# Performance work log

Measured on AMD Instinct MI355X. Metric: run time of the kernel, lower is better.

## Reference

```python
import jax, jax.numpy as jnp
import numpy as np

B, D, P = 8192, 256, 4096
TEMP = 0.5
MOMENTUM = 0.9
EPS = 1e-12  # matches torch F.normalize eps


def _l2_normalize(x):
    n = jnp.sqrt(jnp.sum(x * x, axis=1, keepdims=True))
    return x / jnp.maximum(n, EPS)


def setup_inputs() -> dict:
    key = jax.random.key(0)
    k1, k2, k3 = jax.random.split(key, 3)
    embeddings = jax.random.normal(k1, (B, D), dtype=jnp.float32)
    prototypes = jax.random.normal(k2, (P, D), dtype=jnp.float32)
    cluster_ids = jax.random.randint(k3, (B,), 0, P, dtype=jnp.int64)
    return {"embeddings": embeddings, "prototypes": prototypes, "cluster_ids": cluster_ids}


def reference(embeddings, prototypes, cluster_ids):
    cluster_ids = cluster_ids.astype(jnp.int32)
    emb_norm = _l2_normalize(embeddings)            # [B, D]
    proto_norm = _l2_normalize(prototypes)          # [P, D]
    sim = (emb_norm @ proto_norm.T) / TEMP          # [B, P]

    rows = jnp.arange(sim.shape[0])
    pos_sim = sim[rows, cluster_ids]                # [B]
    neg_sim = sim.at[rows, cluster_ids].set(-jnp.inf)
    # stable logsumexp over negatives (positive column masked out)
    max_val = jnp.max(neg_sim, axis=1, keepdims=True)
    lse = jnp.log(jnp.sum(jnp.exp(neg_sim - max_val), axis=1)) + max_val[:, 0]
    loss = jnp.mean(-pos_sim + lse)

    # serial per-sample EMA prototype update (faithful to the torch for-loop,
    # including sequential dependence on repeated cluster ids)
    def step(protos, xe):
        cid, e = xe
        new_row = MOMENTUM * protos[cid] + (1.0 - MOMENTUM) * e
        return protos.at[cid].set(new_row), None

    new_prototypes, _ = jax.lax.scan(step, prototypes, (cluster_ids, embeddings))
    return loss, new_prototypes
```

## Files before the change

kernel.cpp:

```cpp
#include <hip/hip_runtime.h>
#include <hip/hip_bf16.h>
#include <math.h>

#define Bn 8192
#define Dn 256
#define Pn 4096

using f16x8 = _Float16 __attribute__((ext_vector_type(8)));
using f16x4 = _Float16 __attribute__((ext_vector_type(4)));
using f32x16 = float __attribute__((ext_vector_type(16)));

__global__ void norm_hist_kernel(const float* __restrict__ emb, const float* __restrict__ protos,
                                 const int* __restrict__ cid,
                                 _Float16* __restrict__ embn, _Float16* __restrict__ pron,
                                 float* __restrict__ s_glob, int* __restrict__ hist) {
    __shared__ int h[Pn];
    int gid  = blockIdx.x;
    bool do_hist = (gid < Bn / 256);
    if (do_hist)
        for (int c = threadIdx.x; c < Pn; c += 256) h[c] = 0;

    int row  = gid * 4 + (threadIdx.x >> 6);
    int lane = threadIdx.x & 63;
    const float* in;
    _Float16* out;
    int r;
    if (row < Bn) { in = emb;    out = embn; r = row; }
    else          { in = protos; out = pron; r = row - Bn; }
    const float4 v = reinterpret_cast<const float4*>(in + (size_t)r * Dn)[lane];
    float ss = v.x * v.x + v.y * v.y + v.z * v.z + v.w * v.w;
#pragma unroll
    for (int m = 1; m <= 32; m <<= 1) ss += __shfl_xor(ss, m);
    float scale = 1.0f / fmaxf(sqrtf(ss), 1e-12f);
    f16x4 o;
    o[0] = (_Float16)(v.x * scale);
    o[1] = (_Float16)(v.y * scale);
    o[2] = (_Float16)(v.z * scale);
    o[3] = (_Float16)(v.w * scale);
    reinterpret_cast<f16x4*>(out + (size_t)r * Dn)[lane] = o;

    if (gid < Bn / 1024) s_glob[gid * 256 + threadIdx.x] = 0.0f;

    if (do_hist) {
        __syncthreads();
        atomicAdd(&h[cid[gid * 256 + threadIdx.x]], 1);
        __syncthreads();
        for (int c = threadIdx.x; c < Pn; c += 256)
            hist[gid * Pn + c] = h[c];
    }
}

__global__ __launch_bounds__(1024)
void prefscan_kernel(const int* __restrict__ hist, int* __restrict__ pref,
                     int* __restrict__ offs) {
    __shared__ int wt[16];
    int t = threadIdx.x;
    int4 run = {0, 0, 0, 0};
    for (int ch = 0; ch < 32; ++ch) {
        int4 v = reinterpret_cast<const int4*>(hist + ch * Pn)[t];
        reinterpret_cast<int4*>(pref + ch * Pn)[t] = run;
        run.x += v.x; run.y += v.y; run.z += v.z; run.w += v.w;
    }
    int l1 = run.x, l2 = l1 + run.y, l3 = l2 + run.z;
    int tot = l3 + run.w;
    int v = tot;
#pragma unroll
    for (int d = 1; d < 64; d <<= 1) {
        int u = __shfl_up(v, d);
        if ((t & 63) >= d) v += u;
    }
    if ((t & 63) == 63) wt[t >> 6] = v;
    __syncthreads();
    int add = 0;
    for (int ww = 0; ww < (t >> 6); ++ww) add += wt[ww];
    int base = add + v - tot;
    int4 o = {base, base + l1, base + l2, base + l3};
    reinterpret_cast<int4*>(offs)[t] = o;
    if (t == 0) offs[Pn] = Bn;
}

__global__ void rankfill_kernel(const int* __restrict__ cid, const int* __restrict__ pref,
                                const int* __restrict__ offs, int* __restrict__ slist) {
    __shared__ int ids[256];
    int t = threadIdx.x, g = blockIdx.x;
    int i = g * 256 + t;
    int my = cid[i];
    ids[t] = my;
    __syncthreads();
    int r = pref[g * Pn + my];
    for (int j = 0; j < t; ++j) r += (ids[j] == my) ? 1 : 0;
    slist[offs[my] + r] = i;
}

__global__ __launch_bounds__(256, 2)
void gemm_expsum_kernel(const _Float16* __restrict__ embn, const _Float16* __restrict__ pron,
                        const int* __restrict__ cid,
                        float* __restrict__ s_glob, float* __restrict__ pos_glob) {
    __shared__ _Float16 Bs[2][32 * Dn];
    const int w    = threadIdx.x >> 6;
    const int lane = threadIdx.x & 63;
    const int lo   = lane & 31;
    const int hi   = lane >> 5;
    const int rbase = blockIdx.x * 128 + w * 32;
    const int cbase = blockIdx.y * 256;

    const _Float16* ap = embn + (size_t)(rbase + lo) * Dn + hi * 8;
    f16x8 a[16];
#pragma unroll
    for (int kk = 0; kk < 16; ++kk)
        a[kk] = *reinterpret_cast<const f16x8*>(ap + kk * 16);

    int cidr[16];
#pragma unroll
    for (int r = 0; r < 16; ++r)
        cidr[r] = cid[rbase + (r & 3) + 8 * (r >> 2) + 4 * hi];

    float s[16];
#pragma unroll
    for (int r = 0; r < 16; ++r) s[r] = 0.0f;

    constexpr float K1 = 2.0f * 1.4426950408889634f;

    auto stage = [&](int sub, _Float16* buf) {
#pragma unroll
        for (int i = 0; i < 4; ++i) {
            int g = i * 4 + w;
            const _Float16* gsrc =
                pron + (size_t)(cbase + sub * 32 + lo) * Dn + g * 16 + hi * 8;
            char* l = (char*)buf + (g << 10);
            __builtin_amdgcn_global_load_lds(
                (const __attribute__((address_space(1))) unsigned int*)gsrc,
                (__attribute__((address_space(3))) unsigned int*)l, 16, 0, 0);
        }
    };

    stage(0, Bs[0]);
    __syncthreads();

    for (int sub = 0; sub < 8; ++sub) {
        const _Float16* cur = Bs[sub & 1];
        if (sub < 7) stage(sub + 1, Bs[(sub + 1) & 1]);

        f32x16 acc;
#pragma unroll
        for (int r = 0; r < 16; ++r) acc[r] = 0.0f;
#pragma unroll
        for (int kk = 0; kk < 16; ++kk) {
            f16x8 b = *reinterpret_cast<const f16x8*>(
                (const char*)cur + (kk << 10) + (lane << 4));
            acc = __builtin_amdgcn_mfma_f32_32x32x16_f16(a[kk], b, acc, 0, 0, 0);
        }
        int colv = cbase + sub * 32 + lo;
#pragma unroll
        for (int r = 0; r < 16; ++r) {
            float e = exp2f(fmaf(acc[r], K1, -K1));
            bool ispos = (cidr[r] == colv);
            s[r] += ispos ? 0.0f : e;
            if (ispos)
                pos_glob[rbase + (r & 3) + 8 * (r >> 2) + 4 * hi] = acc[r] * 2.0f;
        }
        __syncthreads();
    }

#pragma unroll
    for (int r = 0; r < 16; ++r) {
        float v = s[r];
        v += __shfl_xor(v, 1);
        v += __shfl_xor(v, 2);
        v += __shfl_xor(v, 4);
        v += __shfl_xor(v, 8);
        v += __shfl_xor(v, 16);
        if (lo == 0) {
            int row = rbase + (r & 3) + 8 * (r >> 2) + 4 * hi;
            atomicAdd(&s_glob[row], v);
        }
    }
}

__global__ void update_loss_kernel(const float* __restrict__ protos, const float* __restrict__ emb,
                                   const int* __restrict__ offs, const int* __restrict__ slist,
                                   const float* __restrict__ s_glob, const float* __restrict__ pos_glob,
                                   float* __restrict__ out) {
    __shared__ float ws2[4];
    float* outp = out + 1;
    int w = threadIdx.x >> 6, lane = threadIdx.x & 63;
    int c = blockIdx.x * 4 + w;
    int off = offs[c], cnt = offs[c + 1] - off;
    float4 p = reinterpret_cast<const float4*>(protos + (size_t)c * Dn)[lane];
    float scale = __powf(0.9f, (float)cnt);
    float4 acc;
    acc.x = p.x * scale; acc.y = p.y * scale; acc.z = p.z * scale; acc.w = p.w * scale;
    for (int j = 0; j < cnt; ++j) {
        int i = slist[off + j];
        float wgt = 0.1f * __powf(0.9f, (float)(cnt - 1 - j));
        float4 e = reinterpret_cast<const float4*>(emb + (size_t)i * Dn)[lane];
        acc.x += wgt * e.x; acc.y += wgt * e.y; acc.z += wgt * e.z; acc.w += wgt * e.w;
    }
    reinterpret_cast<float4*>(outp + (size_t)c * Dn)[lane] = acc;

    if (blockIdx.x == 0) {
        float ssum = 0.0f;
        for (int i = threadIdx.x; i < Bn; i += 256)
            ssum += __logf(s_glob[i]) + 2.0f - pos_glob[i];
#pragma unroll
        for (int m = 1; m <= 32; m <<= 1) ssum += __shfl_xor(ssum, m);
        if ((threadIdx.x & 63) == 0) ws2[threadIdx.x >> 6] = ssum;
        __syncthreads();
        if (threadIdx.x == 0)
            out[0] = (ws2[0] + ws2[1] + ws2[2] + ws2[3]) * (1.0f / (float)Bn);
    }
}

extern "C" void kernel_launch(void* const* d_in, const int* in_sizes, int n_in,
                              void* d_out, int out_size, void* d_ws, size_t ws_size,
                              hipStream_t stream) {
    const float* emb    = (const float*)d_in[0];
    const float* protos = (const float*)d_in[1];
    const int*   cid    = (const int*)d_in[2];
    float* out = (float*)d_out;

    char* ws = (char*)d_ws;
    _Float16* embn = (_Float16*)ws;
    _Float16* pron = (_Float16*)(ws + ((size_t)4 << 20));
    float* s_glob  = (float*)(ws + ((size_t)6 << 20));
    float* pos_g   = (float*)(ws + ((size_t)6 << 20) + 32768);
    int*   offs    = (int*)(ws + ((size_t)6 << 20) + 65536);
    int*   slist   = (int*)(ws + ((size_t)6 << 20) + 98304);
    int*   hist    = (int*)(ws + ((size_t)7 << 20));
    int*   pref    = (int*)(ws + ((size_t)7 << 20) + 524288);

    norm_hist_kernel<<<(Bn + Pn) / 4, 256, 0, stream>>>(emb, protos, cid, embn, pron, s_glob, hist);
    prefscan_kernel<<<1, 1024, 0, stream>>>(hist, pref, offs);
    rankfill_kernel<<<Bn / 256, 256, 0, stream>>>(cid, pref, offs, slist);
    gemm_expsum_kernel<<<dim3(Bn / 128, Pn / 256), 256, 0, stream>>>(embn, pron, cid, s_glob, pos_g);
    update_loss_kernel<<<Pn / 4, 256, 0, stream>>>(protos, emb, offs, slist, s_glob, pos_g, out);
}
```

Measured before the change: 142.3 us.

## Fold softmax scale into embeddings and move positive-column handling out of GEMM

Pre-scales the normalized embeddings by 2/ln2 so the GEMM epilogue is a bare exp2 with no FMA, drops the per-element positive-column mask from the GEMM, and splits the K loop across two independent MFMA accumulators. A new small kernel recomputes the positive dot product, subtracts its exponential from the full sum and writes per-row loss terms. The single-block prefix scan is split into a parallel column-scan kernel and a small offsets kernel, with the GEMM launched earlier. Risks: dropping the max shift relies on bounded cosine similarities, subtracting the positive term can cancel catastrophically, and fp16 rounding of the scaled embedding changes precision slightly.

After: 145.5 us. +2.2%, slower.

```diff
diff --git a/kernel.cpp b/kernel.cpp
--- a/kernel.cpp
+++ b/kernel.cpp
@@ -5,6 +5,9 @@
 #define Bn 8192
 #define Dn 256
 #define Pn 4096
+
+#define SCALE 2.8853900817779268f
+#define LN2   0.6931471805599453f
 
 using f16x8 = _Float16 __attribute__((ext_vector_type(8)));
 using f16x4 = _Float16 __attribute__((ext_vector_type(4)));
@@ -25,13 +28,14 @@
     const float* in;
     _Float16* out;
     int r;
-    if (row < Bn) { in = emb;    out = embn; r = row; }
-    else          { in = protos; out = pron; r = row - Bn; }
+    float post;
+    if (row < Bn) { in = emb;    out = embn; r = row;      post = SCALE; }
+    else          { in = protos; out = pron; r = row - Bn; post = 1.0f;  }
     const float4 v = reinterpret_cast<const float4*>(in + (size_t)r * Dn)[lane];
     float ss = v.x * v.x + v.y * v.y + v.z * v.z + v.w * v.w;
 #pragma unroll
     for (int m = 1; m <= 32; m <<= 1) ss += __shfl_xor(ss, m);
-    float scale = 1.0f / fmaxf(sqrtf(ss), 1e-12f);
+    float scale = post / fmaxf(sqrtf(ss), 1e-12f);
     f16x4 o;
     o[0] = (_Float16)(v.x * scale);
     o[1] = (_Float16)(v.y * scale);
@@ -39,7 +43,7 @@
     o[3] = (_Float16)(v.w * scale);
     reinterpret_cast<f16x4*>(out + (size_t)r * Dn)[lane] = o;
 
-    if (gid < Bn / 1024) s_glob[gid * 256 + threadIdx.x] = 0.0f;
+    if (gid < 32) s_glob[gid * 256 + threadIdx.x] = 0.0f;
 
     if (do_hist) {
         __syncthreads();
@@ -50,32 +54,133 @@
     }
 }
 
-__global__ __launch_bounds__(1024)
-void prefscan_kernel(const int* __restrict__ hist, int* __restrict__ pref,
-                     int* __restrict__ offs) {
-    __shared__ int wt[16];
+__global__ __launch_bounds__(256, 2)
+void gemm_expsum_kernel(const _Float16* __restrict__ embn, const _Float16* __restrict__ pron,
+                        float* __restrict__ s_glob) {
+    __shared__ _Float16 Bs[2][32 * Dn];
+    const int w    = threadIdx.x >> 6;
+    const int lane = threadIdx.x & 63;
+    const int lo   = lane & 31;
+    const int hi   = lane >> 5;
+    const int rbase = blockIdx.x * 128 + w * 32;
+    const int cbase = blockIdx.y * 256;
+
+    const _Float16* ap = embn + (size_t)(rbase + lo) * Dn + hi * 8;
+    f16x8 a[16];
+#pragma unroll
+    for (int kk = 0; kk < 16; ++kk)
+        a[kk] = *reinterpret_cast<const f16x8*>(ap + kk * 16);
+
+    float s[16];
+#pragma unroll
+    for (int r = 0; r < 16; ++r) s[r] = 0.0f;
+
+    auto stage = [&](int sub, _Float16* buf) {
+#pragma unroll
+        for (int i = 0; i < 4; ++i) {
+            int g = i * 4 + w;
+            const _Float16* gsrc =
+                pron + (size_t)(cbase + sub * 32 + lo) * Dn + g * 16 + hi * 8;
+            char* l = (char*)buf + (g << 10);
+            __builtin_amdgcn_global_load_lds(
+                (const __attribute__((address_space(1))) unsigned int*)gsrc,
+                (__attribute__((address_space(3))) unsigned int*)l, 16, 0, 0);
+        }
+    };
+
+    stage(0, Bs[0]);
+    __syncthreads();
+
+    for (int sub = 0; sub < 8; ++sub) {
+        const _Float16* cur = Bs[sub & 1];
+        if (sub < 7) stage(sub + 1, Bs[(sub + 1) & 1]);
+
+        f32x16 acc0, acc1;
+#pragma unroll
+        for (int r = 0; r < 16; ++r) { acc0[r] = 0.0f; acc1[r] = 0.0f; }
+#pragma unroll
+        for (int kk = 0; kk < 16; kk += 2) {
+            f16x8 b0 = *reinterpret_cast<const f16x8*>(
+                (const char*)cur + (kk << 10) + (lane << 4));
+            acc0 = __builtin_amdgcn_mfma_f32_32x32x16_f16(a[kk], b0, acc0, 0, 0, 0);
+            f16x8 b1 = *reinterpret_cast<const f16x8*>(
+                (const char*)cur + ((kk + 1) << 10) + (lane << 4));
+            acc1 = __builtin_amdgcn_mfma_f32_32x32x16_f16(a[kk + 1], b1, acc1, 0, 0, 0);
+        }
+#pragma unroll
+        for (int r = 0; r < 16; ++r)
+            s[r] += exp2f(acc0[r] + acc1[r]);
+
+        __syncthreads();
+    }
+
+#pragma unroll
+    for (int r = 0; r < 16; ++r) {
+        float v = s[r];
+        v += __shfl_xor(v, 1);
+        v += __shfl_xor(v, 2);
+        v += __shfl_xor(v, 4);
+        v += __shfl_xor(v, 8);
+        v += __shfl_xor(v, 16);
+        if (lo == 0) {
+            int row = rbase + (r & 3) + 8 * (r >> 2) + 4 * hi;
+            atomicAdd(&s_glob[row], v);
+        }
+    }
+}
+
+__global__ void loss_terms_kernel(const _Float16* __restrict__ embn, const _Float16* __restrict__ pron,
+                                  const int* __restrict__ cid, const float* __restrict__ s_glob,
+                                  float* __restrict__ terms) {
+    int row  = blockIdx.x * 4 + (threadIdx.x >> 6);
+    int lane = threadIdx.x & 63;
+    int c = cid[row];
+    f16x4 e = reinterpret_cast<const f16x4*>(embn + (size_t)row * Dn)[lane];
+    f16x4 p = reinterpret_cast<const f16x4*>(pron + (size_t)c * Dn)[lane];
+    float d = 0.0f;
+#pragma unroll
+    for (int j = 0; j < 4; ++j) d += (float)e[j] * (float)p[j];
+#pragma unroll
+    for (int m = 1; m <= 32; m <<= 1) d += __shfl_xor(d, m);
+    if (lane == 0) {
+        float accp = d;
+        float sneg = s_glob[row] - exp2f(accp);
+        terms[row] = __logf(sneg) - LN2 * accp;
+    }
+}
+
+__global__ void counts_pref_kernel(const int* __restrict__ hist, int* __restrict__ counts,
+                                   int* __restrict__ pref) {
+    int c = blockIdx.x * 256 + threadIdx.x;
+    int s = 0;
+#pragma unroll
+    for (int ch = 0; ch < 32; ++ch) {
+        pref[ch * Pn + c] = s;
+        s += hist[ch * Pn + c];
+    }
+    counts[c] = s;
+}
+
+__global__ void offsets_kernel(const int* __restrict__ counts, int* __restrict__ offs) {
+    __shared__ int wtot[4];
     int t = threadIdx.x;
-    int4 run = {0, 0, 0, 0};
-    for (int ch = 0; ch < 32; ++ch) {
-        int4 v = reinterpret_cast<const int4*>(hist + ch * Pn)[t];
-        reinterpret_cast<int4*>(pref + ch * Pn)[t] = run;
-        run.x += v.x; run.y += v.y; run.z += v.z; run.w += v.w;
-    }
-    int l1 = run.x, l2 = l1 + run.y, l3 = l2 + run.z;
-    int tot = l3 + run.w;
-    int v = tot;
+    int local[16];
+    int run = 0;
+#pragma unroll
+    for (int j = 0; j < 16; ++j) { local[j] = run; run += counts[t * 16 + j]; }
+    int v = run;
 #pragma unroll
     for (int d = 1; d < 64; d <<= 1) {
         int u = __shfl_up(v, d);
         if ((t & 63) >= d) v += u;
     }
-    if ((t & 63) == 63) wt[t >> 6] = v;
+    if ((t & 63) == 63) wtot[t >> 6] = v;
     __syncthreads();
     int add = 0;
-    for (int ww = 0; ww < (t >> 6); ++ww) add += wt[ww];
-    int base = add + v - tot;
-    int4 o = {base, base + l1, base + l2, base + l3};
-    reinterpret_cast<int4*>(offs)[t] = o;
+    for (int ww = 0; ww < (t >> 6); ++ww) add += wtot[ww];
+    int excl = add + v - run;
+#pragma unroll
+    for (int j = 0; j < 16; ++j) offs[t * 16 + j] = excl + local[j];
     if (t == 0) offs[Pn] = Bn;
 }
 
@@ -92,95 +197,9 @@
     slist[offs[my] + r] = i;
 }
 
-__global__ __launch_bounds__(256, 2)
-void gemm_expsum_kernel(const _Float16* __restrict__ embn, const _Float16* __restrict__ pron,
-                        const int* __restrict__ cid,
-                        float* __restrict__ s_glob, float* __restrict__ pos_glob) {
-    __shared__ _Float16 Bs[2][32 * Dn];
-    const int w    = threadIdx.x >> 6;
-    const int lane = threadIdx.x & 63;
-    const int lo   = lane & 31;
-    const int hi   = lane >> 5;
-    const int rbase = blockIdx.x * 128 + w * 32;
-    const int cbase = blockIdx.y * 256;
-
-    const _Float16* ap = embn + (size_t)(rbase + lo) * Dn + hi * 8;
-    f16x8 a[16];
-#pragma unroll
-    for (int kk = 0; kk < 16; ++kk)
-        a[kk] = *reinterpret_cast<const f16x8*>(ap + kk * 16);
-
-    int cidr[16];
-#pragma unroll
-    for (int r = 0; r < 16; ++r)
-        cidr[r] = cid[rbase + (r & 3) + 8 * (r >> 2) + 4 * hi];
-
-    float s[16];
-#pragma unroll
-    for (int r = 0; r < 16; ++r) s[r] = 0.0f;
-
-    constexpr float K1 = 2.0f * 1.4426950408889634f;
-
-    auto stage = [&](int sub, _Float16* buf) {
-#pragma unroll
-        for (int i = 0; i < 4; ++i) {
-            int g = i * 4 + w;
-            const _Float16* gsrc =
-                pron + (size_t)(cbase + sub * 32 + lo) * Dn + g * 16 + hi * 8;
-            char* l = (char*)buf + (g << 10);
-            __builtin_amdgcn_global_load_lds(
-                (const __attribute__((address_space(1))) unsigned int*)gsrc,
-                (__attribute__((address_space(3))) unsigned int*)l, 16, 0, 0);
-        }
-    };
-
-    stage(0, Bs[0]);
-    __syncthreads();
-
-    for (int sub = 0; sub < 8; ++sub) {
-        const _Float16* cur = Bs[sub & 1];
-        if (sub < 7) stage(sub + 1, Bs[(sub + 1) & 1]);
-
-        f32x16 acc;
-#pragma unroll
-        for (int r = 0; r < 16; ++r) acc[r] = 0.0f;
-#pragma unroll
-        for (int kk = 0; kk < 16; ++kk) {
-            f16x8 b = *reinterpret_cast<const f16x8*>(
-                (const char*)cur + (kk << 10) + (lane << 4));
-            acc = __builtin_amdgcn_mfma_f32_32x32x16_f16(a[kk], b, acc, 0, 0, 0);
-        }
-        int colv = cbase + sub * 32 + lo;
-#pragma unroll
-        for (int r = 0; r < 16; ++r) {
-            float e = exp2f(fmaf(acc[r], K1, -K1));
-            bool ispos = (cidr[r] == colv);
-            s[r] += ispos ? 0.0f : e;
-            if (ispos)
-                pos_glob[rbase + (r & 3) + 8 * (r >> 2) + 4 * hi] = acc[r] * 2.0f;
-        }
-        __syncthreads();
-    }
-
-#pragma unroll
-    for (int r = 0; r < 16; ++r) {
-        float v = s[r];
-        v += __shfl_xor(v, 1);
-        v += __shfl_xor(v, 2);
-        v += __shfl_xor(v, 4);
-        v += __shfl_xor(v, 8);
-        v += __shfl_xor(v, 16);
-        if (lo == 0) {
-            int row = rbase + (r & 3) + 8 * (r >> 2) + 4 * hi;
-            atomicAdd(&s_glob[row], v);
-        }
-    }
-}
-
 __global__ void update_loss_kernel(const float* __restrict__ protos, const float* __restrict__ emb,
                                    const int* __restrict__ offs, const int* __restrict__ slist,
-                                   const float* __restrict__ s_glob, const float* __restrict__ pos_glob,
-                                   float* __restrict__ out) {
+                                   const float* __restrict__ terms, float* __restrict__ out) {
     __shared__ float ws2[4];
     float* outp = out + 1;
     int w = threadIdx.x >> 6, lane = threadIdx.x & 63;
@@ -200,8 +219,7 @@
 
     if (blockIdx.x == 0) {
         float ssum = 0.0f;
-        for (int i = threadIdx.x; i < Bn; i += 256)
-            ssum += __logf(s_glob[i]) + 2.0f - pos_glob[i];
+        for (int i = threadIdx.x; i < Bn; i += 256) ssum += terms[i];
 #pragma unroll
         for (int m = 1; m <= 32; m <<= 1) ssum += __shfl_xor(ssum, m);
         if ((threadIdx.x & 63) == 0) ws2[threadIdx.x >> 6] = ssum;
@@ -223,15 +241,18 @@
     _Float16* embn = (_Float16*)ws;
     _Float16* pron = (_Float16*)(ws + ((size_t)4 << 20));
     float* s_glob  = (float*)(ws + ((size_t)6 << 20));
-    float* pos_g   = (float*)(ws + ((size_t)6 << 20) + 32768);
+    float* terms   = (float*)(ws + ((size_t)6 << 20) + 32768);
     int*   offs    = (int*)(ws + ((size_t)6 << 20) + 65536);
     int*   slist   = (int*)(ws + ((size_t)6 << 20) + 98304);
+    int*   counts  = (int*)(ws + ((size_t)6 << 20) + 131072);
     int*   hist    = (int*)(ws + ((size_t)7 << 20));
     int*   pref    = (int*)(ws + ((size_t)7 << 20) + 524288);
 
     norm_hist_kernel<<<(Bn + Pn) / 4, 256, 0, stream>>>(emb, protos, cid, embn, pron, s_glob, hist);
-    prefscan_kernel<<<1, 1024, 0, stream>>>(hist, pref, offs);
+    gemm_expsum_kernel<<<dim3(Bn / 128, Pn / 256), 256, 0, stream>>>(embn, pron, s_glob);
+    loss_terms_kernel<<<Bn / 4, 256, 0, stream>>>(embn, pron, cid, s_glob, terms);
+    counts_pref_kernel<<<Pn / 256, 256, 0, stream>>>(hist, counts, pref);
+    offsets_kernel<<<1, 256, 0, stream>>>(counts, offs);
     rankfill_kernel<<<Bn / 256, 256, 0, stream>>>(cid, pref, offs, slist);
-    gemm_expsum_kernel<<<dim3(Bn / 128, Pn / 256), 256, 0, stream>>>(embn, pron, cid, s_glob, pos_g);
-    update_loss_kernel<<<Pn / 4, 256, 0, stream>>>(protos, emb, offs, slist, s_glob, pos_g, out);
-}
+    update_loss_kernel<<<Pn / 4, 256, 0, stream>>>(protos, emb, offs, slist, terms, out);
+}
```
